# Kernel tuning notes

Measured on AMD Instinct MI355X. Metric: run time of the kernel, lower is better.

The kernel has to match this reference:

```python
import jax, jax.numpy as jnp
from jax import lax
import numpy as np

B = 8; L = 1024; D_MODEL = 128; N_LAYER = 4
D_INNER = 256; D_STATE = 16; D_CONV = 4; DT_RANK = 8  # ceil(128/16)
N_STATE = 2; EPS = 1e-5


def setup_inputs() -> dict:
    key = jax.random.key(0)
    ks = jax.random.split(key, 9)
    s = 0.02
    return {
        "x": jax.random.normal(ks[0], (B, L, D_MODEL), jnp.float32),
        "in_proj_w": jax.random.normal(ks[1], (N_LAYER, 2 * D_INNER, D_MODEL), jnp.float32) * s,
        "conv_w": jax.random.normal(ks[2], (N_LAYER, D_INNER, 1, D_CONV), jnp.float32) * s,
        "conv_b": jnp.zeros((N_LAYER, D_INNER), jnp.float32),
        "x_proj_w": jax.random.normal(ks[3], (N_LAYER, DT_RANK + 2 * D_STATE, D_INNER), jnp.float32) * s,
        "dt_proj_w": jax.random.normal(ks[4], (N_LAYER, D_INNER, DT_RANK), jnp.float32) * s,
        "dt_proj_b": jax.random.normal(ks[5], (N_LAYER, D_INNER), jnp.float32) * s,
        "A_log": jnp.log(jnp.tile(jnp.arange(1, D_STATE + 1, dtype=jnp.float32), (N_LAYER, D_INNER, 1))),
        "D_param": jnp.ones((N_LAYER, D_INNER), jnp.float32),
        "out_proj_w": jax.random.normal(ks[6], (N_LAYER, D_MODEL, D_INNER), jnp.float32) * s,
        "norm_w": jnp.ones((N_LAYER, D_MODEL), jnp.float32),
        "norm_f_w": jnp.ones((D_MODEL,), jnp.float32),
        "bn_gamma": jnp.ones((D_MODEL,), jnp.float32),
        "bn_beta": jnp.zeros((D_MODEL,), jnp.float32),
        "head_w": jax.random.normal(ks[7], (N_STATE, D_MODEL), jnp.float32) * s,
        "head_b": jnp.zeros((N_STATE,), jnp.float32),
    }


def _rmsnorm(x, w):
    return x * lax.rsqrt(jnp.mean(x * x, axis=-1, keepdims=True) + EPS) * w


def _selective_scan(u, delta, A, Bm, Cm, D):
    # u, delta: (b,l,d); A: (d,n); Bm, Cm: (b,l,n); D: (d,)
    deltaA = jnp.exp(delta[..., None] * A)                          # (b,l,d,n)
    deltaBu = delta[..., None] * Bm[:, :, None, :] * u[..., None]   # (b,l,d,n)

    def step(h, t):
        dA, dBu, c = t
        h = dA * h + dBu                                            # (b,d,n)
        return h, jnp.einsum('bdn,bn->bd', h, c)

    h0 = jnp.zeros((u.shape[0], u.shape[2], A.shape[1]), u.dtype)
    _, ys = lax.scan(step, h0, (jnp.moveaxis(deltaA, 1, 0),
                                jnp.moveaxis(deltaBu, 1, 0),
                                jnp.moveaxis(Cm, 1, 0)))
    return jnp.moveaxis(ys, 0, 1) + u * D                           # (b,l,d)


def _mamba_block(x, in_w, cw, cb, xp_w, dt_w, dt_b, A_log, Dp, out_w):
    xz = jnp.einsum('bld,ed->ble', x, in_w)                         # (b,l,2*d_inner)
    xs, res = jnp.split(xz, 2, axis=-1)
    # depthwise causal conv, kernel D_CONV, left pad D_CONV-1 (matches pad=3 + truncate)
    xc = lax.conv_general_dilated(jnp.transpose(xs, (0, 2, 1)), cw, (1,),
                                  [(D_CONV - 1, 0)],
                                  dimension_numbers=('NCH', 'OIH', 'NCH'),
                                  feature_group_count=D_INNER)
    xs = jax.nn.silu(jnp.transpose(xc + cb[None, :, None], (0, 2, 1)))
    dbc = jnp.einsum('bld,ed->ble', xs, xp_w)
    dlt, Bm, Cm = jnp.split(dbc, [DT_RANK, DT_RANK + D_STATE], axis=-1)
    delta = jax.nn.softplus(jnp.einsum('blr,dr->bld', dlt, dt_w) + dt_b)
    A = -jnp.exp(A_log)
    y = _selective_scan(xs, delta, A, Bm, Cm, Dp)
    y = y * jax.nn.silu(res)
    return jnp.einsum('ble,de->bld', y, out_w)


def reference(x, in_proj_w, conv_w, conv_b, x_proj_w, dt_proj_w, dt_proj_b,
              A_log, D_param, out_proj_w, norm_w, norm_f_w,
              bn_gamma, bn_beta, head_w, head_b):
    h = x
    for i in range(N_LAYER):
        h = h + _mamba_block(_rmsnorm(h, norm_w[i]), in_proj_w[i], conv_w[i],
                             conv_b[i], x_proj_w[i], dt_proj_w[i], dt_proj_b[i],
                             A_log[i], D_param[i], out_proj_w[i])
    h = _rmsnorm(h, norm_f_w)
    feat = h[:, -1, :]                                              # (b, d_model)
    # BatchNorm1d (training mode: batch stats, biased variance), ReLU, Dropout(eval)=id
    mu = jnp.mean(feat, axis=0)
    var = jnp.mean((feat - mu) ** 2, axis=0)
    feat = (feat - mu) * lax.rsqrt(var + EPS) * bn_gamma + bn_beta
    feat = jax.nn.relu(feat)
    return feat @ head_w.T + head_b                                 # (b, n_state)
```

## Files before the change

### kernel.cpp

```cpp
#include <hip/hip_runtime.h>
#include <cstddef>

#define LQ 1024
#define DM 128
#define DI 256
#define DSN 16
#define NB 8
#define ROWS (NB*LQ)
#define EPSF 1e-5f
#define CHUNK 16
#define NCHUNK (LQ/CHUNK)

typedef _Float16 f16;
typedef __attribute__((ext_vector_type(8))) _Float16 f16x8;
typedef __attribute__((ext_vector_type(4))) _Float16 f16x4;
typedef __attribute__((ext_vector_type(4))) float f32x4;

static __device__ __forceinline__ float sigmoid_f(float x) { return 1.f/(1.f+__expf(-x)); }
static __device__ __forceinline__ float softplus_f(float x) {
  return (x > 20.f) ? x : log1pf(__expf(x));
}

__global__ __launch_bounds__(256) void cvt_all(
    const float* __restrict__ a, const float* __restrict__ bsrc, const float* __restrict__ csrc,
    f16* __restrict__ oa, f16* __restrict__ ob, f16* __restrict__ oc)
{
  int i = blockIdx.x*256 + threadIdx.x;
  const int na = (4*2*DI*DM)/4;
  const int nb = (4*40*DI)/4;
  const int nc = (4*DM*DI)/4;
  const float* s; f16* o; int k;
  if (i < na)            { s = a;    o = oa; k = i; }
  else if (i < na+nb)    { s = bsrc; o = ob; k = i - na; }
  else if (i < na+nb+nc) { s = csrc; o = oc; k = i - na - nb; }
  else return;
  float4 v = ((const float4*)s)[k];
  f16x4 r; r.x=(f16)v.x; r.y=(f16)v.y; r.z=(f16)v.z; r.w=(f16)v.w;
  ((f16x4*)o)[k] = r;
}

__global__ __launch_bounds__(256) void norm_inproj(
    const float* __restrict__ hin, const float* __restrict__ nw,
    const f16* __restrict__ Wf, f16* __restrict__ xz)
{
  __shared__ __align__(16) f16 Alds[64][136];
  __shared__ __align__(16) f16 Blds[64][136];
  const int tid = threadIdx.x;
  const int row0 = blockIdx.x*64, col0 = blockIdx.y*64;
  #pragma unroll
  for (int cc = tid; cc < 1024; cc += 256) {
    int r = cc >> 4, off = (cc & 15) << 3;
    *(f16x8*)&Blds[r][off] = *(const f16x8*)(Wf + (size_t)(col0 + r)*DM + off);
  }
  {
    const int r = tid >> 2, seg = (tid & 3) * 32;
    const float* hr = hin + (size_t)(row0 + r)*DM + seg;
    float4 v[8];
    float ss = 0.f;
    #pragma unroll
    for (int j = 0; j < 8; ++j) {
      v[j] = *(const float4*)(hr + j*4);
      ss += v[j].x*v[j].x + v[j].y*v[j].y + v[j].z*v[j].z + v[j].w*v[j].w;
    }
    ss += __shfl_xor(ss, 1);
    ss += __shfl_xor(ss, 2);
    const float sc = rsqrtf(ss*(1.f/128.f) + EPSF);
    #pragma unroll
    for (int j = 0; j < 8; ++j) {
      float4 wv = *(const float4*)(nw + seg + j*4);
      f16x4 o;
      o.x = (f16)(v[j].x*sc*wv.x);
      o.y = (f16)(v[j].y*sc*wv.y);
      o.z = (f16)(v[j].z*sc*wv.z);
      o.w = (f16)(v[j].w*sc*wv.w);
      *(f16x4*)&Alds[r][seg + j*4] = o;
    }
  }
  __syncthreads();
  const int l = tid & 63, w = tid >> 6;
  const int wr = w >> 1, wc = w & 1;
  const int fr = l & 15, kg = l >> 4;
  f16x8 af[2][4], bf[2][4];
  #pragma unroll
  for (int m = 0; m < 2; ++m)
    #pragma unroll
    for (int s = 0; s < 4; ++s)
      af[m][s] = *(const f16x8*)&Alds[wr*32 + m*16 + fr][s*32 + kg*8];
  #pragma unroll
  for (int n = 0; n < 2; ++n)
    #pragma unroll
    for (int s = 0; s < 4; ++s)
      bf[n][s] = *(const f16x8*)&Blds[wc*32 + n*16 + fr][s*32 + kg*8];
  f32x4 acc[2][2];
  #pragma unroll
  for (int m = 0; m < 2; ++m)
    #pragma unroll
    for (int n = 0; n < 2; ++n)
      acc[m][n] = (f32x4){0.f,0.f,0.f,0.f};
  #pragma unroll
  for (int s = 0; s < 4; ++s)
    #pragma unroll
    for (int m = 0; m < 2; ++m)
      #pragma unroll
      for (int n = 0; n < 2; ++n)
        acc[m][n] = __builtin_amdgcn_mfma_f32_16x16x32_f16(af[m][s], bf[n][s], acc[m][n], 0, 0, 0);
  #pragma unroll
  for (int m = 0; m < 2; ++m)
    #pragma unroll
    for (int n = 0; n < 2; ++n) {
      const int col = col0 + wc*32 + n*16 + fr;
      #pragma unroll
      for (int j = 0; j < 4; ++j) {
        const int row = row0 + wr*32 + m*16 + kg*4 + j;
        xz[(size_t)row*(2*DI) + col] = (f16)acc[m][n][j];
      }
    }
}

__global__ __launch_bounds__(256) void layer_front(
    const f16* __restrict__ xz, const float* __restrict__ cw, const float* __restrict__ cb,
    const f16* __restrict__ xpw, const float* __restrict__ A_log,
    const float* __restrict__ dtw, const float* __restrict__ dtb,
    f16* __restrict__ xs_out, float* __restrict__ dbc_out,
    float* __restrict__ S, float* __restrict__ sumdl_out)
{
  __shared__ __align__(16) f16 sXz[19][264];
  __shared__ __align__(16) f16 sXs[16][264];
  __shared__ __align__(16) float sDbc[16][40];
  const int bc = blockIdx.x;
  const int b = bc >> 6, ck = bc & (NCHUNK-1);
  const int t0 = ck*CHUNK;
  const int tid = threadIdx.x;
  const int l = tid & 63, w = tid >> 6;
  const int fr = l & 15, kg = l >> 4;

  for (int e = tid; e < 19*32; e += 256) {
    int r = e >> 5, off = (e & 31) << 3;
    f16x8 v = (f16x8){0,0,0,0,0,0,0,0};
    if (ck > 0 || r >= 3)
      v = *(const f16x8*)(xz + (size_t)(b*LQ + t0 - 3 + r)*(2*DI) + off);
    *(f16x8*)&sXz[r][off] = v;
  }
  __syncthreads();

  {
    const int d = tid;
    const float4 cwv = *(const float4*)(cw + d*4);
    const float bias = cb[d];
    #pragma unroll 4
    for (int t = 0; t < CHUNK; ++t) {
      float a = bias + (float)sXz[t][d]*cwv.x + (float)sXz[t+1][d]*cwv.y
                     + (float)sXz[t+2][d]*cwv.z + (float)sXz[t+3][d]*cwv.w;
      float sv = a * sigmoid_f(a);
      f16 s16 = (f16)sv;
      sXs[t][d] = s16;
      xs_out[(size_t)(b*LQ + t0 + t)*DI + d] = s16;
    }
  }
  __syncthreads();

  if (w < 3) {
    const int col = w*16 + fr;
    f32x4 acc = (f32x4){0.f,0.f,0.f,0.f};
    #pragma unroll
    for (int s = 0; s < 8; ++s) {
      f16x8 bfv = (f16x8){0,0,0,0,0,0,0,0};
      if (col < 40) bfv = *(const f16x8*)(xpw + (size_t)col*DI + s*32 + kg*8);
      f16x8 afv = *(const f16x8*)&sXs[fr][s*32 + kg*8];
      acc = __builtin_amdgcn_mfma_f32_16x16x32_f16(afv, bfv, acc, 0, 0, 0);
    }
    if (col < 40) {
      #pragma unroll
      for (int j = 0; j < 4; ++j) {
        int row = kg*4 + j;
        sDbc[row][col] = acc[j];
        dbc_out[(size_t)(b*LQ + t0 + row)*40 + col] = acc[j];
      }
    }
  }
  __syncthreads();

  {
    const int d = tid;
    float A[16];
    #pragma unroll
    for (int n = 0; n < 16; ++n) A[n] = -__expf(A_log[d*16+n]);
    const float4 dw0 = *(const float4*)(dtw + d*8);
    const float4 dw1 = *(const float4*)(dtw + d*8 + 4);
    const float bt = dtb[d];
    float h[16] = {};
    float sdl = 0.f;
    for (int t = 0; t < CHUNK; ++t) {
      float xa = bt + sDbc[t][0]*dw0.x + sDbc[t][1]*dw0.y + sDbc[t][2]*dw0.z + sDbc[t][3]*dw0.w
                    + sDbc[t][4]*dw1.x + sDbc[t][5]*dw1.y + sDbc[t][6]*dw1.z + sDbc[t][7]*dw1.w;
      float dl = softplus_f(xa);
      float du = dl * (float)sXs[t][d];
      sdl += dl;
      #pragma unroll
      for (int n = 0; n < 16; ++n)
        h[n] = __expf(dl*A[n])*h[n] + du*sDbc[t][8+n];
    }
    float* Sp = S + ((size_t)bc*DI + d)*16;
    #pragma unroll
    for (int n = 0; n < 16; n += 4)
      *(float4*)(Sp+n) = make_float4(h[n],h[n+1],h[n+2],h[n+3]);
    sumdl_out[(size_t)bc*DI + d] = sdl;
  }
}

__global__ __launch_bounds__(256) void scan_p2(
    float* __restrict__ S, const float* __restrict__ sumdl,
    const float* __restrict__ A_log)
{
  int g = blockIdx.x*256 + threadIdx.x;
  int b = g >> 12;
  int dn = g & 4095;
  float A = -__expf(A_log[dn]);
  int d = dn >> 4;
  float H = 0.f;
  for (int c = 0; c < NCHUNK; ++c) {
    size_t cidx = (size_t)(b*NCHUNK + c)*DI + d;
    size_t idx = cidx*16 + (dn & 15);
    float Sv = S[idx];
    float P = __expf(A * sumdl[cidx]);
    S[idx] = H;
    H = P*H + Sv;
  }
}

__global__ __launch_bounds__(256) void layer_back(
    const f16* __restrict__ xs, const float* __restrict__ dbc,
    const float* __restrict__ A_log, const float* __restrict__ dtw,
    const float* __restrict__ dtb, const float* __restrict__ Dp,
    const float* __restrict__ Hinit, const f16* __restrict__ xz,
    const f16* __restrict__ Wo, const float* __restrict__ addsrc,
    float* __restrict__ hout)
{
  __shared__ __align__(16) f16 sXs[16][264];
  __shared__ __align__(16) f16 sZ[16][264];
  __shared__ __align__(16) f16 sY[16][264];
  __shared__ __align__(16) float sDbc[16][40];
  const int bc = blockIdx.x;
  const int b = bc >> 6, ck = bc & (NCHUNK-1);
  const int t0 = ck*CHUNK;
  const int tid = threadIdx.x;
  const int l = tid & 63, w = tid >> 6;
  const int fr = l & 15, kg = l >> 4;

  {
    const int r = tid >> 4, col = (tid & 15) * 16;
    *(f16x8*)&sXs[r][col]   = *(const f16x8*)(xs + (size_t)(b*LQ + t0 + r)*DI + col);
    *(f16x8*)&sXs[r][col+8] = *(const f16x8*)(xs + (size_t)(b*LQ + t0 + r)*DI + col + 8);
    *(f16x8*)&sZ[r][col]    = *(const f16x8*)(xz + (size_t)(b*LQ + t0 + r)*(2*DI) + DI + col);
    *(f16x8*)&sZ[r][col+8]  = *(const f16x8*)(xz + (size_t)(b*LQ + t0 + r)*(2*DI) + DI + col + 8);
  }
  for (int e = tid; e < 16*40; e += 256) {
    int t = e / 40, c = e % 40;
    sDbc[t][c] = dbc[(size_t)(b*LQ + t0 + t)*40 + c];
  }

  const int d = tid;
  float A[16];
  #pragma unroll
  for (int n = 0; n < 16; ++n) A[n] = -__expf(A_log[d*16+n]);
  float h[16];
  {
    const float* Hp = Hinit + ((size_t)bc*DI + d)*16;
    #pragma unroll
    for (int n = 0; n < 16; n += 4) {
      float4 v = *(const float4*)(Hp+n);
      h[n]=v.x; h[n+1]=v.y; h[n+2]=v.z; h[n+3]=v.w;
    }
  }
  const float4 dw0 = *(const float4*)(dtw + d*8);
  const float4 dw1 = *(const float4*)(dtw + d*8 + 4);
  const float bt = dtb[d];
  const float Dv = Dp[d];

  f16x8 bf[2][8];
  #pragma unroll
  for (int n = 0; n < 2; ++n)
    #pragma unroll
    for (int s = 0; s < 8; ++s)
      bf[n][s] = *(const f16x8*)(Wo + (size_t)(w*32 + n*16 + fr)*DI + s*32 + kg*8);
  __syncthreads();

  for (int t = 0; t < CHUNK; ++t) {
    float xa = bt + sDbc[t][0]*dw0.x + sDbc[t][1]*dw0.y + sDbc[t][2]*dw0.z + sDbc[t][3]*dw0.w
                  + sDbc[t][4]*dw1.x + sDbc[t][5]*dw1.y + sDbc[t][6]*dw1.z + sDbc[t][7]*dw1.w;
    float dl = softplus_f(xa);
    float uu = (float)sXs[t][d];
    float du = dl*uu;
    float pacc = uu*Dv;
    #pragma unroll
    for (int n = 0; n < 16; ++n) {
      h[n] = __expf(dl*A[n])*h[n] + du*sDbc[t][8+n];
      pacc += h[n]*sDbc[t][24+n];
    }
    float res = (float)sZ[t][d];
    sY[t][d] = (f16)(pacc * (res * sigmoid_f(res)));
  }
  __syncthreads();

  {
    f32x4 acc[2];
    acc[0] = (f32x4){0.f,0.f,0.f,0.f};
    acc[1] = (f32x4){0.f,0.f,0.f,0.f};
    #pragma unroll
    for (int s = 0; s < 8; ++s) {
      f16x8 afv = *(const f16x8*)&sY[fr][s*32 + kg*8];
      #pragma unroll
      for (int n = 0; n < 2; ++n)
        acc[n] = __builtin_amdgcn_mfma_f32_16x16x32_f16(afv, bf[n][s], acc[n], 0, 0, 0);
    }
    #pragma unroll
    for (int n = 0; n < 2; ++n) {
      const int col = w*32 + n*16 + fr;
      #pragma unroll
      for (int j = 0; j < 4; ++j) {
        const int row = kg*4 + j;
        const size_t gi = (size_t)(b*LQ + t0 + row)*DM + col;
        hout[gi] = acc[n][j] + addsrc[gi];
      }
    }
  }
}

__global__ __launch_bounds__(256) void final_kernel(const float* __restrict__ h,
    const float* __restrict__ nfw, const float* __restrict__ gamma, const float* __restrict__ beta,
    const float* __restrict__ hw, const float* __restrict__ hb, float* __restrict__ out) {
  __shared__ float sf[8][128];
  __shared__ float sscale[8];
  int tid = threadIdx.x;
  for (int e = tid; e < 1024; e += 256) {
    int b = e >> 7, dd = e & 127;
    sf[b][dd] = h[((size_t)b*LQ + (LQ-1))*DM + dd];
  }
  __syncthreads();
  if (tid < 8) {
    float ss = 0.f;
    for (int dd = 0; dd < 128; ++dd) { float v = sf[tid][dd]; ss += v*v; }
    sscale[tid] = rsqrtf(ss/128.f + EPSF);
  }
  __syncthreads();
  for (int e = tid; e < 1024; e += 256) {
    int b = e >> 7, dd = e & 127;
    sf[b][dd] = sf[b][dd]*sscale[b]*nfw[dd];
  }
  __syncthreads();
  if (tid < 128) {
    float mu = 0.f;
    for (int b = 0; b < 8; ++b) mu += sf[b][tid];
    mu *= 0.125f;
    float var = 0.f;
    for (int b = 0; b < 8; ++b) { float dv = sf[b][tid]-mu; var += dv*dv; }
    var *= 0.125f;
    float rs = rsqrtf(var + EPSF);
    for (int b = 0; b < 8; ++b) {
      float v = (sf[b][tid]-mu)*rs*gamma[tid] + beta[tid];
      sf[b][tid] = v > 0.f ? v : 0.f;
    }
  }
  __syncthreads();
  if (tid < 16) {
    int b = tid >> 1, s = tid & 1;
    float acc = hb[s];
    for (int dd = 0; dd < 128; ++dd) acc += sf[b][dd]*hw[s*128+dd];
    out[b*2+s] = acc;
  }
}

extern "C" void kernel_launch(void* const* d_in, const int* in_sizes, int n_in,
                              void* d_out, int out_size, void* d_ws, size_t ws_size,
                              hipStream_t stream) {
  const float* x      = (const float*)d_in[0];
  const float* in_w   = (const float*)d_in[1];
  const float* conv_w = (const float*)d_in[2];
  const float* conv_b = (const float*)d_in[3];
  const float* xp_w   = (const float*)d_in[4];
  const float* dt_w   = (const float*)d_in[5];
  const float* dt_b   = (const float*)d_in[6];
  const float* A_log  = (const float*)d_in[7];
  const float* Dp     = (const float*)d_in[8];
  const float* out_w  = (const float*)d_in[9];
  const float* norm_w = (const float*)d_in[10];
  const float* norm_f = (const float*)d_in[11];
  const float* gamma  = (const float*)d_in[12];
  const float* beta   = (const float*)d_in[13];
  const float* head_w = (const float*)d_in[14];
  const float* head_b = (const float*)d_in[15];

  float* ws = (float*)d_ws;
  float* h     = ws;
  float* dbc   = h + (size_t)ROWS*DM;
  float* S     = dbc + (size_t)ROWS*40;
  float* sumdl = S + (size_t)NB*NCHUNK*DI*16;
  f16* xz     = (f16*)(sumdl + (size_t)NB*NCHUNK*DI);
  f16* xs     = xz + (size_t)ROWS*2*DI;
  f16* wf_in  = xs + (size_t)ROWS*DI;
  f16* wf_xp  = wf_in + (size_t)4*2*DI*DM;
  f16* wf_out = wf_xp + (size_t)4*40*DI;

  cvt_all<<<424, 256, 0, stream>>>(in_w, xp_w, out_w, wf_in, wf_xp, wf_out);

  for (int layer = 0; layer < 4; ++layer) {
    const float* src = layer ? h : x;
    norm_inproj<<<dim3(ROWS/64, 8), 256, 0, stream>>>(
        src, norm_w + (size_t)layer*DM, wf_in + (size_t)layer*2*DI*DM, xz);
    layer_front<<<NB*NCHUNK, 256, 0, stream>>>(
        xz, conv_w + (size_t)layer*DI*4, conv_b + (size_t)layer*DI,
        wf_xp + (size_t)layer*40*DI, A_log + (size_t)layer*DI*DSN,
        dt_w + (size_t)layer*DI*8, dt_b + (size_t)layer*DI,
        xs, dbc, S, sumdl);
    scan_p2<<<NB*DI*DSN/256, 256, 0, stream>>>(S, sumdl, A_log + (size_t)layer*DI*DSN);
    layer_back<<<NB*NCHUNK, 256, 0, stream>>>(
        xs, dbc, A_log + (size_t)layer*DI*DSN, dt_w + (size_t)layer*DI*8,
        dt_b + (size_t)layer*DI, Dp + (size_t)layer*DI, S, xz,
        wf_out + (size_t)layer*DM*DI, src, h);
  }
  final_kernel<<<1, 256, 0, stream>>>(h, norm_f, gamma, beta, head_w, head_b, (float*)d_out);
}
```

Measured before the change: 285.3 us.

## Fuse RMSNorm and in_proj GEMM into scan front and back kernels

Removes the standalone norm_inproj kernel and the f16 xz intermediate buffer. layer_front now normalizes the chunk's input rows, including 3 halo rows, and computes the x-half of in_proj with MFMA straight into shared memory. layer_back recomputes the norm for its 16 rows and computes the z-half of in_proj itself. This drops one launch per layer and the global write and read of xz. In exchange both kernels do extra GEMM work, some halo rows are recomputed, and in_proj weights are read from global memory by every block.

After: 261.5 us. 8.3% less time.

```diff
diff --git a/kernel.cpp b/kernel.cpp
--- a/kernel.cpp
+++ b/kernel.cpp
@@ -10,6 +10,7 @@
 #define EPSF 1e-5f
 #define CHUNK 16
 #define NCHUNK (LQ/CHUNK)
+#define NBLK (NB*NCHUNK)
 
 typedef _Float16 f16;
 typedef __attribute__((ext_vector_type(8))) _Float16 f16x8;
@@ -39,92 +40,18 @@
   ((f16x4*)o)[k] = r;
 }
 
-__global__ __launch_bounds__(256) void norm_inproj(
-    const float* __restrict__ hin, const float* __restrict__ nw,
-    const f16* __restrict__ Wf, f16* __restrict__ xz)
-{
-  __shared__ __align__(16) f16 Alds[64][136];
-  __shared__ __align__(16) f16 Blds[64][136];
-  const int tid = threadIdx.x;
-  const int row0 = blockIdx.x*64, col0 = blockIdx.y*64;
-  #pragma unroll
-  for (int cc = tid; cc < 1024; cc += 256) {
-    int r = cc >> 4, off = (cc & 15) << 3;
-    *(f16x8*)&Blds[r][off] = *(const f16x8*)(Wf + (size_t)(col0 + r)*DM + off);
-  }
-  {
-    const int r = tid >> 2, seg = (tid & 3) * 32;
-    const float* hr = hin + (size_t)(row0 + r)*DM + seg;
-    float4 v[8];
-    float ss = 0.f;
-    #pragma unroll
-    for (int j = 0; j < 8; ++j) {
-      v[j] = *(const float4*)(hr + j*4);
-      ss += v[j].x*v[j].x + v[j].y*v[j].y + v[j].z*v[j].z + v[j].w*v[j].w;
-    }
-    ss += __shfl_xor(ss, 1);
-    ss += __shfl_xor(ss, 2);
-    const float sc = rsqrtf(ss*(1.f/128.f) + EPSF);
-    #pragma unroll
-    for (int j = 0; j < 8; ++j) {
-      float4 wv = *(const float4*)(nw + seg + j*4);
-      f16x4 o;
-      o.x = (f16)(v[j].x*sc*wv.x);
-      o.y = (f16)(v[j].y*sc*wv.y);
-      o.z = (f16)(v[j].z*sc*wv.z);
-      o.w = (f16)(v[j].w*sc*wv.w);
-      *(f16x4*)&Alds[r][seg + j*4] = o;
-    }
-  }
-  __syncthreads();
-  const int l = tid & 63, w = tid >> 6;
-  const int wr = w >> 1, wc = w & 1;
-  const int fr = l & 15, kg = l >> 4;
-  f16x8 af[2][4], bf[2][4];
-  #pragma unroll
-  for (int m = 0; m < 2; ++m)
-    #pragma unroll
-    for (int s = 0; s < 4; ++s)
-      af[m][s] = *(const f16x8*)&Alds[wr*32 + m*16 + fr][s*32 + kg*8];
-  #pragma unroll
-  for (int n = 0; n < 2; ++n)
-    #pragma unroll
-    for (int s = 0; s < 4; ++s)
-      bf[n][s] = *(const f16x8*)&Blds[wc*32 + n*16 + fr][s*32 + kg*8];
-  f32x4 acc[2][2];
-  #pragma unroll
-  for (int m = 0; m < 2; ++m)
-    #pragma unroll
-    for (int n = 0; n < 2; ++n)
-      acc[m][n] = (f32x4){0.f,0.f,0.f,0.f};
-  #pragma unroll
-  for (int s = 0; s < 4; ++s)
-    #pragma unroll
-    for (int m = 0; m < 2; ++m)
-      #pragma unroll
-      for (int n = 0; n < 2; ++n)
-        acc[m][n] = __builtin_amdgcn_mfma_f32_16x16x32_f16(af[m][s], bf[n][s], acc[m][n], 0, 0, 0);
-  #pragma unroll
-  for (int m = 0; m < 2; ++m)
-    #pragma unroll
-    for (int n = 0; n < 2; ++n) {
-      const int col = col0 + wc*32 + n*16 + fr;
-      #pragma unroll
-      for (int j = 0; j < 4; ++j) {
-        const int row = row0 + wr*32 + m*16 + kg*4 + j;
-        xz[(size_t)row*(2*DI) + col] = (f16)acc[m][n][j];
-      }
-    }
-}
-
 __global__ __launch_bounds__(256) void layer_front(
-    const f16* __restrict__ xz, const float* __restrict__ cw, const float* __restrict__ cb,
-    const f16* __restrict__ xpw, const float* __restrict__ A_log,
+    const float* __restrict__ src, const float* __restrict__ nw,
+    const f16* __restrict__ Win,
+    const float* __restrict__ cw, const float* __restrict__ cb,
+    const f16* __restrict__ xpw,
+    const float* __restrict__ A_log,
     const float* __restrict__ dtw, const float* __restrict__ dtb,
     f16* __restrict__ xs_out, float* __restrict__ dbc_out,
     float* __restrict__ S, float* __restrict__ sumdl_out)
 {
-  __shared__ __align__(16) f16 sXz[19][264];
+  __shared__ __align__(16) f16 Ah[19][136];
+  __shared__ __align__(16) f16 sXc[19][264];
   __shared__ __align__(16) f16 sXs[16][264];
   __shared__ __align__(16) float sDbc[16][40];
   const int bc = blockIdx.x;
@@ -134,12 +61,71 @@
   const int l = tid & 63, w = tid >> 6;
   const int fr = l & 15, kg = l >> 4;
 
-  for (int e = tid; e < 19*32; e += 256) {
-    int r = e >> 5, off = (e & 31) << 3;
-    f16x8 v = (f16x8){0,0,0,0,0,0,0,0};
-    if (ck > 0 || r >= 3)
-      v = *(const f16x8*)(xz + (size_t)(b*LQ + t0 - 3 + r)*(2*DI) + off);
-    *(f16x8*)&sXz[r][off] = v;
+  {
+    const int r = tid >> 3;
+    const int seg = (tid & 7) * 16;
+    const bool valid = (r < 19) && (ck > 0 || r >= 3);
+    float4 v[4];
+    float ss = 0.f;
+    if (valid) {
+      const float* hr = src + (size_t)(b*LQ + t0 - 3 + r)*DM + seg;
+      #pragma unroll
+      for (int j = 0; j < 4; ++j) {
+        v[j] = *(const float4*)(hr + j*4);
+        ss += v[j].x*v[j].x + v[j].y*v[j].y + v[j].z*v[j].z + v[j].w*v[j].w;
+      }
+    }
+    ss += __shfl_xor(ss, 1); ss += __shfl_xor(ss, 2); ss += __shfl_xor(ss, 4);
+    if (r < 19) {
+      if (valid) {
+        const float sc = rsqrtf(ss*(1.f/128.f) + EPSF);
+        #pragma unroll
+        for (int j = 0; j < 4; ++j) {
+          float4 wv = *(const float4*)(nw + seg + j*4);
+          f16x4 o;
+          o.x=(f16)(v[j].x*sc*wv.x); o.y=(f16)(v[j].y*sc*wv.y);
+          o.z=(f16)(v[j].z*sc*wv.z); o.w=(f16)(v[j].w*sc*wv.w);
+          *(f16x4*)&Ah[r][seg + j*4] = o;
+        }
+      } else {
+        #pragma unroll
+        for (int j = 0; j < 4; ++j)
+          *(f16x4*)&Ah[r][seg + j*4] = (f16x4){0,0,0,0};
+      }
+    }
+  }
+  __syncthreads();
+
+  {
+    f32x4 ax1[4], ax2[4];
+    #pragma unroll
+    for (int n = 0; n < 4; ++n) {
+      ax1[n] = (f32x4){0.f,0.f,0.f,0.f};
+      ax2[n] = (f32x4){0.f,0.f,0.f,0.f};
+    }
+    #pragma unroll
+    for (int s = 0; s < 4; ++s) {
+      f16x8 a1 = *(const f16x8*)&Ah[fr][s*32 + kg*8];
+      f16x8 a2 = *(const f16x8*)&Ah[3 + fr][s*32 + kg*8];
+      #pragma unroll
+      for (int n = 0; n < 4; ++n) {
+        f16x8 bx = *(const f16x8*)(Win + (size_t)(w*64 + n*16 + fr)*DM + s*32 + kg*8);
+        ax1[n] = __builtin_amdgcn_mfma_f32_16x16x32_f16(a1, bx, ax1[n], 0, 0, 0);
+        ax2[n] = __builtin_amdgcn_mfma_f32_16x16x32_f16(a2, bx, ax2[n], 0, 0, 0);
+      }
+    }
+    #pragma unroll
+    for (int n = 0; n < 4; ++n) {
+      const int col = w*64 + n*16 + fr;
+      #pragma unroll
+      for (int j = 0; j < 4; ++j)
+        sXc[3 + kg*4 + j][col] = (f16)ax2[n][j];
+      if (kg == 0) {
+        #pragma unroll
+        for (int j = 0; j < 3; ++j)
+          sXc[j][col] = (f16)ax1[n][j];
+      }
+    }
   }
   __syncthreads();
 
@@ -149,8 +135,8 @@
     const float bias = cb[d];
     #pragma unroll 4
     for (int t = 0; t < CHUNK; ++t) {
-      float a = bias + (float)sXz[t][d]*cwv.x + (float)sXz[t+1][d]*cwv.y
-                     + (float)sXz[t+2][d]*cwv.z + (float)sXz[t+3][d]*cwv.w;
+      float a = bias + (float)sXc[t][d]*cwv.x + (float)sXc[t+1][d]*cwv.y
+                     + (float)sXc[t+2][d]*cwv.z + (float)sXc[t+3][d]*cwv.w;
       float sv = a * sigmoid_f(a);
       f16 s16 = (f16)sv;
       sXs[t][d] = s16;
@@ -229,13 +215,15 @@
 }
 
 __global__ __launch_bounds__(256) void layer_back(
+    const float* __restrict__ src, const float* __restrict__ nw,
+    const f16* __restrict__ Win,
     const f16* __restrict__ xs, const float* __restrict__ dbc,
     const float* __restrict__ A_log, const float* __restrict__ dtw,
     const float* __restrict__ dtb, const float* __restrict__ Dp,
-    const float* __restrict__ Hinit, const f16* __restrict__ xz,
-    const f16* __restrict__ Wo, const float* __restrict__ addsrc,
+    const float* __restrict__ Hinit, const f16* __restrict__ Wo,
     float* __restrict__ hout)
 {
+  __shared__ __align__(16) f16 Ah[16][136];
   __shared__ __align__(16) f16 sXs[16][264];
   __shared__ __align__(16) f16 sZ[16][264];
   __shared__ __align__(16) f16 sY[16][264];
@@ -251,12 +239,54 @@
     const int r = tid >> 4, col = (tid & 15) * 16;
     *(f16x8*)&sXs[r][col]   = *(const f16x8*)(xs + (size_t)(b*LQ + t0 + r)*DI + col);
     *(f16x8*)&sXs[r][col+8] = *(const f16x8*)(xs + (size_t)(b*LQ + t0 + r)*DI + col + 8);
-    *(f16x8*)&sZ[r][col]    = *(const f16x8*)(xz + (size_t)(b*LQ + t0 + r)*(2*DI) + DI + col);
-    *(f16x8*)&sZ[r][col+8]  = *(const f16x8*)(xz + (size_t)(b*LQ + t0 + r)*(2*DI) + DI + col + 8);
   }
   for (int e = tid; e < 16*40; e += 256) {
     int t = e / 40, c = e % 40;
     sDbc[t][c] = dbc[(size_t)(b*LQ + t0 + t)*40 + c];
+  }
+  {
+    const int r = tid >> 4;
+    const int seg = (tid & 15) * 8;
+    const float* hr = src + (size_t)(b*LQ + t0 + r)*DM + seg;
+    float4 v0 = *(const float4*)(hr);
+    float4 v1 = *(const float4*)(hr + 4);
+    float ss = v0.x*v0.x+v0.y*v0.y+v0.z*v0.z+v0.w*v0.w
+             + v1.x*v1.x+v1.y*v1.y+v1.z*v1.z+v1.w*v1.w;
+    ss += __shfl_xor(ss, 1); ss += __shfl_xor(ss, 2);
+    ss += __shfl_xor(ss, 4); ss += __shfl_xor(ss, 8);
+    const float sc = rsqrtf(ss*(1.f/128.f) + EPSF);
+    float4 w0 = *(const float4*)(nw + seg);
+    float4 w1 = *(const float4*)(nw + seg + 4);
+    f16x4 o0, o1;
+    o0.x=(f16)(v0.x*sc*w0.x); o0.y=(f16)(v0.y*sc*w0.y);
+    o0.z=(f16)(v0.z*sc*w0.z); o0.w=(f16)(v0.w*sc*w0.w);
+    o1.x=(f16)(v1.x*sc*w1.x); o1.y=(f16)(v1.y*sc*w1.y);
+    o1.z=(f16)(v1.z*sc*w1.z); o1.w=(f16)(v1.w*sc*w1.w);
+    *(f16x4*)&Ah[r][seg]   = o0;
+    *(f16x4*)&Ah[r][seg+4] = o1;
+  }
+  __syncthreads();
+
+  {
+    f32x4 az[4];
+    #pragma unroll
+    for (int n = 0; n < 4; ++n) az[n] = (f32x4){0.f,0.f,0.f,0.f};
+    #pragma unroll
+    for (int s = 0; s < 4; ++s) {
+      f16x8 a = *(const f16x8*)&Ah[fr][s*32 + kg*8];
+      #pragma unroll
+      for (int n = 0; n < 4; ++n) {
+        f16x8 bz = *(const f16x8*)(Win + (size_t)(DI + w*64 + n*16 + fr)*DM + s*32 + kg*8);
+        az[n] = __builtin_amdgcn_mfma_f32_16x16x32_f16(a, bz, az[n], 0, 0, 0);
+      }
+    }
+    #pragma unroll
+    for (int n = 0; n < 4; ++n) {
+      const int col = w*64 + n*16 + fr;
+      #pragma unroll
+      for (int j = 0; j < 4; ++j)
+        sZ[kg*4 + j][col] = (f16)az[n][j];
+    }
   }
 
   const int d = tid;
@@ -276,7 +306,6 @@
   const float4 dw1 = *(const float4*)(dtw + d*8 + 4);
   const float bt = dtb[d];
   const float Dv = Dp[d];
-
   f16x8 bf[2][8];
   #pragma unroll
   for (int n = 0; n < 2; ++n)
@@ -320,7 +349,7 @@
       for (int j = 0; j < 4; ++j) {
         const int row = kg*4 + j;
         const size_t gi = (size_t)(b*LQ + t0 + row)*DM + col;
-        hout[gi] = acc[n][j] + addsrc[gi];
+        hout[gi] = acc[n][j] + src[gi];
       }
     }
   }
@@ -395,8 +424,7 @@
   float* dbc   = h + (size_t)ROWS*DM;
   float* S     = dbc + (size_t)ROWS*40;
   float* sumdl = S + (size_t)NB*NCHUNK*DI*16;
-  f16* xz     = (f16*)(sumdl + (size_t)NB*NCHUNK*DI);
-  f16* xs     = xz + (size_t)ROWS*2*DI;
+  f16* xs     = (f16*)(sumdl + (size_t)NB*NCHUNK*DI);
   f16* wf_in  = xs + (size_t)ROWS*DI;
   f16* wf_xp  = wf_in + (size_t)4*2*DI*DM;
   f16* wf_out = wf_xp + (size_t)4*40*DI;
@@ -405,18 +433,19 @@
 
   for (int layer = 0; layer < 4; ++layer) {
     const float* src = layer ? h : x;
-    norm_inproj<<<dim3(ROWS/64, 8), 256, 0, stream>>>(
-        src, norm_w + (size_t)layer*DM, wf_in + (size_t)layer*2*DI*DM, xz);
-    layer_front<<<NB*NCHUNK, 256, 0, stream>>>(
-        xz, conv_w + (size_t)layer*DI*4, conv_b + (size_t)layer*DI,
+    layer_front<<<NBLK, 256, 0, stream>>>(
+        src, norm_w + (size_t)layer*DM, wf_in + (size_t)layer*2*DI*DM,
+        conv_w + (size_t)layer*DI*4, conv_b + (size_t)layer*DI,
         wf_xp + (size_t)layer*40*DI, A_log + (size_t)layer*DI*DSN,
         dt_w + (size_t)layer*DI*8, dt_b + (size_t)layer*DI,
         xs, dbc, S, sumdl);
     scan_p2<<<NB*DI*DSN/256, 256, 0, stream>>>(S, sumdl, A_log + (size_t)layer*DI*DSN);
-    layer_back<<<NB*NCHUNK, 256, 0, stream>>>(
-        xs, dbc, A_log + (size_t)layer*DI*DSN, dt_w + (size_t)layer*DI*8,
-        dt_b + (size_t)layer*DI, Dp + (size_t)layer*DI, S, xz,
-        wf_out + (size_t)layer*DM*DI, src, h);
+    layer_back<<<NBLK, 256, 0, stream>>>(
+        src, norm_w + (size_t)layer*DM, wf_in + (size_t)layer*2*DI*DM,
+        xs, dbc, A_log + (size_t)layer*DI*DSN,
+        dt_w + (size_t)layer*DI*8, dt_b + (size_t)layer*DI,
+        Dp + (size_t)layer*DI, S,
+        wf_out + (size_t)layer*DM*DI, h);
   }
   final_kernel<<<1, 256, 0, stream>>>(h, norm_f, gamma, beta, head_w, head_b, (float*)d_out);
 }
```
